# Kernel tuning notes

Hardware: AMD Instinct MI355X
Metric: run time of the kernel (lower is better)

The kernel has to match this reference:

```python
import jax, jax.numpy as jnp
import numpy as np

B = 64  # batch_size (number of graphs)


def _leaky(v):
    return jax.nn.leaky_relu(v, 0.01)


def _gine(x, src, dst, edge_attr, ew, eb, w1, b1, w2, b2):
    # GINEConv (eps=0): out = nn(x + sum_{j->i} relu(x_j + lin(edge_attr)))
    n = x.shape[0]
    msg = jax.nn.relu(x[src] + edge_attr @ ew + eb)      # [E, C]
    agg = jax.ops.segment_sum(msg, dst, num_segments=n)  # [N, C]
    h = x + agg
    h = _leaky(h @ w1 + b1)
    h = _leaky(h @ w2 + b2)
    return h


def setup_inputs() -> dict:
    key = jax.random.key(0)
    ks = jax.random.split(key, 32)
    N, E, NF, EF, H, A = 65536, 1048576, 32, 16, 128, 10
    s = 0.05
    inp = {
        'x': jax.random.normal(ks[0], (N, NF), jnp.float32),
        'edge_index': jax.random.randint(ks[1], (2, E), 0, N, jnp.int64)
        if jax.config.jax_enable_x64 else jax.random.randint(ks[1], (2, E), 0, N, jnp.int32),
        'edge_attr': jax.random.normal(ks[2], (E, EF), jnp.float32),
        'e1_w': jax.random.normal(ks[3], (EF, NF)) * s, 'e1_b': jnp.zeros((NF,)),
        'c1_w1': jax.random.normal(ks[4], (NF, H)) * s, 'c1_b1': jnp.zeros((H,)),
        'c1_w2': jax.random.normal(ks[5], (H, H)) * s, 'c1_b2': jnp.zeros((H,)),
        'e2_w': jax.random.normal(ks[6], (EF, H)) * s, 'e2_b': jnp.zeros((H,)),
        'c2_w1': jax.random.normal(ks[7], (H, H)) * s, 'c2_b1': jnp.zeros((H,)),
        'c2_w2': jax.random.normal(ks[8], (H, H)) * s, 'c2_b2': jnp.zeros((H,)),
        'a_w1': jax.random.normal(ks[9], (H, H)) * s, 'a_b1': jnp.zeros((H,)),
        'a_w2': jax.random.normal(ks[10], (H, A)) * s, 'a_b2': jnp.zeros((A,)),
        'n_w1': jax.random.normal(ks[11], (H, H)) * s, 'n_b1': jnp.zeros((H,)),
        'n_w2': jax.random.normal(ks[12], (H, H)) * s, 'n_b2': jnp.zeros((H,)),
        'n_w3': jax.random.normal(ks[13], (H, 1)) * s, 'n_b3': jnp.zeros((1,)),
    }
    return inp


def reference(x, edge_index, edge_attr,
              e1_w, e1_b, c1_w1, c1_b1, c1_w2, c1_b2,
              e2_w, e2_b, c2_w1, c2_b1, c2_w2, c2_b2,
              a_w1, a_b1, a_w2, a_b2,
              n_w1, n_b1, n_w2, n_b2, n_w3, n_b3):
    src, dst = edge_index[0], edge_index[1]
    h = _gine(x, src, dst, edge_attr, e1_w, e1_b, c1_w1, c1_b1, c1_w2, c1_b2)
    h = jax.nn.relu(h)  # dropout is identity in eval mode
    h = _gine(h, src, dst, edge_attr, e2_w, e2_b, c2_w1, c2_b1, c2_w2, c2_b2)
    H = h.shape[-1]
    hb = h.reshape(B, -1, H)            # [B, Nper, H]
    pooled = hb.mean(axis=1)            # [B, H]
    a = _leaky(_leaky(pooled @ a_w1 + a_b1) @ a_w2 + a_b2)
    action_prob = jax.nn.softmax(a, axis=1)
    # reinterpret flat node order as [Nper, B, H], as in the torch reshape
    xr = h.reshape(-1, B, H)
    nh = _leaky(xr @ n_w1 + n_b1)
    nh = _leaky(nh @ n_w2 + n_b2)
    node_scores = jax.nn.sigmoid(nh @ n_w3 + n_b3)[..., 0].T  # [B, Nper]
    return action_prob, node_scores
```

## Files before the change

kernel.cpp:

```cpp
#include <hip/hip_runtime.h>
#include <math.h>

#define NNODES 65536
#define NEDGES 1048576
#define NF 32
#define EF 16
#define HD 128
#define NACT 10
#define NB 64
#define NPER 1024

typedef unsigned short u16;
typedef float  vf2  __attribute__((ext_vector_type(2)));
typedef float  vf4  __attribute__((ext_vector_type(4)));
typedef __bf16 vbf8 __attribute__((ext_vector_type(8)));
#define BC8(v) __builtin_bit_cast(vbf8, v)
#define WB() __builtin_amdgcn_wave_barrier()

__device__ __forceinline__ float leakyf(float v) { return v > 0.0f ? v : 0.01f * v; }
__device__ __forceinline__ vf2 fma2(vf2 a, vf2 b, vf2 c) { return __builtin_elementwise_fma(a, b, c); }
__device__ __forceinline__ vf2 max2(vf2 a, vf2 b) { return __builtin_elementwise_max(a, b); }
__device__ __forceinline__ vf2 splat2(float s) { vf2 r = {s, s}; return r; }

__device__ __forceinline__ u16 f2bf(float x) {
    unsigned u = __float_as_uint(x);
    return (u16)((u + 0x7FFFu + ((u >> 16) & 1u)) >> 16);
}
__device__ __forceinline__ float bf2f(u16 h) { return __uint_as_float(((unsigned)h) << 16); }

__device__ __forceinline__ vf2 up2(unsigned d) {
    vf2 r = { __uint_as_float(d << 16), __uint_as_float(d & 0xFFFF0000u) };
    return r;
}

__device__ __forceinline__ void cvt4(const float4 s, uint2& hi, uint2& lo) {
    const u16 h0 = f2bf(s.x), h1 = f2bf(s.y), h2 = f2bf(s.z), h3 = f2bf(s.w);
    hi = make_uint2((unsigned)h0 | ((unsigned)h1 << 16), (unsigned)h2 | ((unsigned)h3 << 16));
    const u16 l0 = f2bf(s.x - bf2f(h0)), l1 = f2bf(s.y - bf2f(h1));
    const u16 l2 = f2bf(s.z - bf2f(h2)), l3 = f2bf(s.w - bf2f(h3));
    lo = make_uint2((unsigned)l0 | ((unsigned)l1 << 16), (unsigned)l2 | ((unsigned)l3 << 16));
}
__device__ __forceinline__ uint2 cvt4hi(const float4 s) {
    const u16 h0 = f2bf(s.x), h1 = f2bf(s.y), h2 = f2bf(s.z), h3 = f2bf(s.w);
    return make_uint2((unsigned)h0 | ((unsigned)h1 << 16), (unsigned)h2 | ((unsigned)h3 << 16));
}

template<int K>
__device__ __forceinline__ void bcast16_fma(const float av, const vf2* __restrict__ wr, vf2& m) {
    const float a = __uint_as_float((unsigned)__builtin_amdgcn_ds_swizzle(
        (int)__float_as_uint(av), (K << 5) | 0x10));
    m = fma2(splat2(a), wr[K], m);
    if constexpr (K + 1 < EF) bcast16_fma<K + 1>(av, wr, m);
}

__global__ __launch_bounds__(256) void hist_kernel(const int* __restrict__ ei, int* __restrict__ cnt)
{
    const int i = blockIdx.x * 256 + threadIdx.x;
    if (i < NEDGES) atomicAdd(&cnt[ei[NEDGES + i]], 1);
}

__global__ __launch_bounds__(1024) void scan_kernel(const int* __restrict__ cnt, int* __restrict__ rs)
{
    __shared__ int s[1024];
    const int t = threadIdx.x;
    int loc[64];
    int tot = 0;
    const int4* c4 = (const int4*)(cnt + t * 64);
    #pragma unroll
    for (int j = 0; j < 16; ++j) {
        const int4 v = c4[j];
        loc[4*j+0] = v.x; loc[4*j+1] = v.y; loc[4*j+2] = v.z; loc[4*j+3] = v.w;
        tot += v.x + v.y + v.z + v.w;
    }
    s[t] = tot;
    __syncthreads();
    for (int off = 1; off < 1024; off <<= 1) {
        const int v = (t >= off) ? s[t - off] : 0;
        __syncthreads();
        s[t] += v;
        __syncthreads();
    }
    int run = s[t] - tot;
    #pragma unroll
    for (int j = 0; j < 64; ++j) { rs[t * 64 + j] = run; run += loc[j]; }
    if (t == 0) rs[NNODES] = NEDGES;
}

__global__ __launch_bounds__(256) void scatter_kernel(
    const int* __restrict__ ei, const int* __restrict__ rs, int* __restrict__ fill,
    int* __restrict__ ssrc, int* __restrict__ seidx)
{
    const int i = blockIdx.x * 256 + threadIdx.x;
    if (i < NEDGES) {
        const int d = ei[NEDGES + i];
        const int pos = rs[d] + atomicAdd(&fill[d], 1);
        ssrc[pos]  = ei[i];
        seidx[pos] = i;
    }
}

__global__ __launch_bounds__(256) void permute_kernel(
    const int* __restrict__ seidx, const float* __restrict__ ea, float* __restrict__ sea)
{
    const int t = blockIdx.x * 256 + threadIdx.x;
    const int e = t >> 2, part = t & 3;
    const int idx = seidx[e];
    ((float4*)sea)[(size_t)e * 4 + part] = ((const float4*)ea)[(size_t)idx * 4 + part];
}

__global__ __launch_bounds__(256) void pack_all_kernel(
    const float* __restrict__ w0, const float* __restrict__ w1, const float* __restrict__ w2,
    const float* __restrict__ w3, const float* __restrict__ w4, const float* __restrict__ w5,
    u16* __restrict__ pw)
{
    const int bid = blockIdx.x;
    const float* W; int KB, seg, sbase;
    if (bid < 16) { W = w0; KB = 1; seg = 0; sbase = 0; }
    else {
        const int i = (bid - 16) >> 6;
        seg = i + 1; sbase = 16 + i * 64; KB = 4;
        W = (i == 0) ? w1 : (i == 1) ? w2 : (i == 2) ? w3 : (i == 3) ? w4 : w5;
    }
    const int t = (bid - sbase) * 256 + threadIdx.x;
    const int j = t & 7, lane = (t >> 3) & 63, rest = t >> 9;
    const int kb = rest % KB, fb = rest / KB;
    if (fb >= 8) return;
    const int k = kb * 32 + (lane >> 4) * 8 + j;
    const int f = fb * 16 + (lane & 15);
    const float val = W[k * HD + f];
    const u16 h = f2bf(val);
    u16* dst = pw + seg * 32768;
    dst[t] = h;
    dst[16384 + t] = f2bf(val - bf2f(h));
}

__global__ __launch_bounds__(256) void e1_agg_kernel(
    const float* __restrict__ x, const int* __restrict__ rs,
    const int* __restrict__ ssrc, const float* __restrict__ sea,
    const float* __restrict__ w, const float* __restrict__ b, float* __restrict__ agg)
{
    const int tid  = threadIdx.x;
    const int lane = tid & 63;
    const int p    = lane & 15;
    const int q    = lane >> 4;
    const int node0 = (blockIdx.x * 4 + (tid >> 6)) * 4;
    vf2 wr[EF];
    #pragma unroll
    for (int k = 0; k < EF; ++k) wr[k] = *(const vf2*)&w[k * NF + p * 2];
    const vf2 bias = *(const vf2*)&b[p * 2];
    int rsv[5];
    #pragma unroll
    for (int i = 0; i < 5; ++i) rsv[i] = __builtin_amdgcn_readfirstlane(rs[node0 + i]);
    int srcLn[4];
    #pragma unroll
    for (int n = 0; n < 4; ++n) {
        const int nw0 = min(rsv[n + 1] - rsv[n], 64);
        srcLn[n] = (lane < nw0) ? ssrc[rsv[n] + lane] : 0;
    }
    #pragma unroll
    for (int n = 0; n < 4; ++n) {
        const int beg = rsv[n], end = rsv[n + 1];
        vf2 acc = {0.0f, 0.0f};
        int srcL = srcLn[n];
        for (int wnd = beg; wnd < end; wnd += 64) {
            const int nw = min(end - wnd, 64);
            if (wnd != beg) srcL = (lane < nw) ? ssrc[wnd + lane] : 0;
            const float* sbase = sea + (size_t)wnd * EF;
            int blk = 0;
            for (; blk + 16 <= nw; blk += 16) {
                float av[4];
                #pragma unroll
                for (int u = 0; u < 4; ++u)
                    av[u] = sbase[blk * EF + u * 64 + lane];
                vf2 xv[4];
                #pragma unroll
                for (int u = 0; u < 4; ++u) {
                    const int sA = __shfl(srcL, blk + u * 4 + q, 64);
                    xv[u] = *(const vf2*)((const char*)x + (((unsigned)sA << 7) + (unsigned)p * 8));
                }
                #pragma unroll
                for (int u = 0; u < 4; ++u) {
                    vf2 m = bias;
                    bcast16_fma<0>(av[u], wr, m);
                    acc += max2(xv[u] + m, splat2(0.0f));
                }
            }
            const int nrem = nw - blk;
            if (nrem > 0) {
                #pragma unroll
                for (int u = 0; u < 4; ++u) {
                    if (u * 4 >= nrem) break;
                    const int myidx = u * 4 + q;
                    const bool valid = myidx < nrem;
                    const float av = valid ? sbase[blk * EF + u * 64 + lane] : 0.0f;
                    const int sA = __shfl(srcL, min(blk + myidx, nw - 1), 64);
                    const vf2 xv = *(const vf2*)((const char*)x + (((unsigned)sA << 7) + (unsigned)p * 8));
                    vf2 m = bias;
                    bcast16_fma<0>(av, wr, m);
                    if (valid) acc += max2(xv + m, splat2(0.0f));
                }
            }
        }
        acc[0] += __shfl_xor(acc[0], 16, 64); acc[1] += __shfl_xor(acc[1], 16, 64);
        acc[0] += __shfl_xor(acc[0], 32, 64); acc[1] += __shfl_xor(acc[1], 32, 64);
        if (lane < 16) *(vf2*)&agg[(size_t)(node0 + n) * NF + p * 2] = acc;
    }
}

__global__ __launch_bounds__(256) void e2_agg_kernel(
    const u16* __restrict__ h16, const int* __restrict__ rs,
    const int* __restrict__ ssrc, const float* __restrict__ sea,
    const float* __restrict__ w, const float* __restrict__ b, float* __restrict__ agg)
{
    const int tid  = threadIdx.x;
    const int lane = tid & 63;
    const unsigned foff = (unsigned)lane * 4;
    const int node = blockIdx.x * 4 + (tid >> 6);
    vf2 wr[EF];
    #pragma unroll
    for (int k = 0; k < EF; ++k) wr[k] = *(const vf2*)&w[k * HD + lane * 2];
    const vf2 bias = *(const vf2*)&b[lane * 2];
    const int beg = __builtin_amdgcn_readfirstlane(rs[node]);
    const int end = __builtin_amdgcn_readfirstlane(rs[node + 1]);
    vf2 acc = {0.0f, 0.0f};
    int e = beg;
    #define LDH(s) (*(const unsigned*)((const char*)h16 + (((unsigned)(s) << 8) + foff)))
    if (e + 4 <= end) {
        int s0 = ssrc[e], s1 = ssrc[e + 1], s2 = ssrc[e + 2], s3 = ssrc[e + 3];
        unsigned d0 = LDH(s0), d1 = LDH(s1), d2 = LDH(s2), d3 = LDH(s3);
        for (; e + 8 <= end; e += 4) {
            const int t0 = ssrc[e + 4], t1 = ssrc[e + 5], t2 = ssrc[e + 6], t3 = ssrc[e + 7];
            const unsigned g0 = LDH(t0), g1 = LDH(t1), g2 = LDH(t2), g3 = LDH(t3);
            const float* a0 = &sea[(size_t)e * EF];
            vf2 m0 = bias, m1 = bias, m2 = bias, m3 = bias;
            #pragma unroll
            for (int k = 0; k < EF; ++k) {
                m0 = fma2(splat2(a0[k]),      wr[k], m0);
                m1 = fma2(splat2(a0[16 + k]), wr[k], m1);
            }
            acc += max2(up2(d0) + m0, splat2(0.0f));
            acc += max2(up2(d1) + m1, splat2(0.0f));
            #pragma unroll
            for (int k = 0; k < EF; ++k) {
                m2 = fma2(splat2(a0[32 + k]), wr[k], m2);
                m3 = fma2(splat2(a0[48 + k]), wr[k], m3);
            }
            acc += max2(up2(d2) + m2, splat2(0.0f));
            acc += max2(up2(d3) + m3, splat2(0.0f));
            s0 = t0; s1 = t1; s2 = t2; s3 = t3;
            d0 = g0; d1 = g1; d2 = g2; d3 = g3;
        }
        {
            const float* a0 = &sea[(size_t)e * EF];
            vf2 m0 = bias, m1 = bias, m2 = bias, m3 = bias;
            #pragma unroll
            for (int k = 0; k < EF; ++k) {
                m0 = fma2(splat2(a0[k]),      wr[k], m0);
                m1 = fma2(splat2(a0[16 + k]), wr[k], m1);
            }
            acc += max2(up2(d0) + m0, splat2(0.0f));
            acc += max2(up2(d1) + m1, splat2(0.0f));
            #pragma unroll
            for (int k = 0; k < EF; ++k) {
                m2 = fma2(splat2(a0[32 + k]), wr[k], m2);
                m3 = fma2(splat2(a0[48 + k]), wr[k], m3);
            }
            acc += max2(up2(d2) + m2, splat2(0.0f));
            acc += max2(up2(d3) + m3, splat2(0.0f));
            e += 4;
        }
    }
    for (; e < end; ++e) {
        const int sA = ssrc[e];
        const unsigned dA = LDH(sA);
        const float* aA = &sea[(size_t)e * EF];
        vf2 mA = bias;
        #pragma unroll
        for (int k = 0; k < EF; ++k) mA = fma2(splat2(aA[k]), wr[k], mA);
        acc += max2(up2(dA) + mA, splat2(0.0f));
    }
    #undef LDH
    *(vf2*)&agg[(size_t)node * HD + lane * 2] = acc;
}

#define ROW128 272
#define ROW32  80

__device__ __forceinline__ void mfma_layer128_in(
    const unsigned char* __restrict__ aH, const unsigned char* __restrict__ aL,
    const u16* __restrict__ wH, const u16* __restrict__ wL,
    const float* __restrict__ bias, int lane, vf4* __restrict__ acc)
{
    const int quad = lane >> 4, fm = lane & 15;
    int4 Bh[4], Bl[4];
    #pragma unroll
    for (int kb = 0; kb < 4; ++kb) {
        Bh[kb] = *(const int4*)(aH + fm * ROW128 + kb * 64 + quad * 16);
        Bl[kb] = *(const int4*)(aL + fm * ROW128 + kb * 64 + quad * 16);
    }
    #pragma unroll
    for (int fb = 0; fb < 8; ++fb) {
        const float4 bv = *(const float4*)&bias[fb * 16 + quad * 4];
        vf4 a = {bv.x, bv.y, bv.z, bv.w};
        #pragma unroll
        for (int kb = 0; kb < 4; ++kb) {
            const int4 wh = *(const int4*)(wH + ((fb * 4 + kb) * 64 + lane) * 8);
            const int4 wl = *(const int4*)(wL + ((fb * 4 + kb) * 64 + lane) * 8);
            a = __builtin_amdgcn_mfma_f32_16x16x32_bf16(BC8(wh), BC8(Bl[kb]), a, 0, 0, 0);
            a = __builtin_amdgcn_mfma_f32_16x16x32_bf16(BC8(wl), BC8(Bh[kb]), a, 0, 0, 0);
            a = __builtin_amdgcn_mfma_f32_16x16x32_bf16(BC8(wh), BC8(Bh[kb]), a, 0, 0, 0);
        }
        acc[fb] = a;
    }
}

__device__ __forceinline__ void mfma_layer128_act(
    const unsigned char* __restrict__ aH,
    const u16* __restrict__ wH, const u16* __restrict__ wL,
    const float* __restrict__ bias, int lane, vf4* __restrict__ acc)
{
    const int quad = lane >> 4, fm = lane & 15;
    int4 Bh[4];
    #pragma unroll
    for (int kb = 0; kb < 4; ++kb)
        Bh[kb] = *(const int4*)(aH + fm * ROW128 + kb * 64 + quad * 16);
    #pragma unroll
    for (int fb = 0; fb < 8; ++fb) {
        const float4 bv = *(const float4*)&bias[fb * 16 + quad * 4];
        vf4 a = {bv.x, bv.y, bv.z, bv.w};
        #pragma unroll
        for (int kb = 0; kb < 4; ++kb) {
            const int4 wh = *(const int4*)(wH + ((fb * 4 + kb) * 64 + lane) * 8);
            const int4 wl = *(const int4*)(wL + ((fb * 4 + kb) * 64 + lane) * 8);
            a = __builtin_amdgcn_mfma_f32_16x16x32_bf16(BC8(wl), BC8(Bh[kb]), a, 0, 0, 0);
            a = __builtin_amdgcn_mfma_f32_16x16x32_bf16(BC8(wh), BC8(Bh[kb]), a, 0, 0, 0);
        }
        acc[fb] = a;
    }
}

__device__ __forceinline__ void mfma_layer32_in(
    const unsigned char* __restrict__ aH, const unsigned char* __restrict__ aL,
    const u16* __restrict__ wH, const u16* __restrict__ wL,
    const float* __restrict__ bias, int lane, vf4* __restrict__ acc)
{
    const int quad = lane >> 4, fm = lane & 15;
    const int4 Bh = *(const int4*)(aH + fm * ROW32 + quad * 16);
    const int4 Bl = *(const int4*)(aL + fm * ROW32 + quad * 16);
    #pragma unroll
    for (int fb = 0; fb < 8; ++fb) {
        const float4 bv = *(const float4*)&bias[fb * 16 + quad * 4];
        vf4 a = {bv.x, bv.y, bv.z, bv.w};
        const int4 wh = *(const int4*)(wH + (fb * 64 + lane) * 8);
        const int4 wl = *(const int4*)(wL + (fb * 64 + lane) * 8);
        a = __builtin_amdgcn_mfma_f32_16x16x32_bf16(BC8(wh), BC8(Bl), a, 0, 0, 0);
        a = __builtin_amdgcn_mfma_f32_16x16x32_bf16(BC8(wl), BC8(Bh), a, 0, 0, 0);
        a = __builtin_amdgcn_mfma_f32_16x16x32_bf16(BC8(wh), BC8(Bh), a, 0, 0, 0);
        acc[fb] = a;
    }
}

__device__ __forceinline__ void store_act_hi(
    unsigned char* __restrict__ aH, int lane, vf4* __restrict__ acc)
{
    const int quad = lane >> 4, fm = lane & 15;
    #pragma unroll
    for (int fb = 0; fb < 8; ++fb) {
        const float4 s = {leakyf(acc[fb][0]), leakyf(acc[fb][1]), leakyf(acc[fb][2]), leakyf(acc[fb][3])};
        acc[fb][0] = s.x; acc[fb][1] = s.y; acc[fb][2] = s.z; acc[fb][3] = s.w;
        *(uint2*)(aH + fm * ROW128 + fb * 32 + quad * 8) = cvt4hi(s);
    }
}

__global__ __launch_bounds__(256) void n1_kernel(
    const float* __restrict__ x, const float* __restrict__ agg,
    const u16* __restrict__ w1h, const u16* __restrict__ w1l, const float* __restrict__ b1,
    const u16* __restrict__ w2h, const u16* __restrict__ w2l, const float* __restrict__ b2,
    float* __restrict__ hout, u16* __restrict__ hb16)
{
    __shared__ __align__(16) unsigned char smem[4][2560 + 16 * ROW128];
    const int tid = threadIdx.x, lane = tid & 63, wid = tid >> 6;
    const int quad = lane >> 4, fm = lane & 15;
    const int tile = blockIdx.x * 4 + wid;
    unsigned char* inH = smem[wid];
    unsigned char* inL = inH + 16 * ROW32;
    unsigned char* aH  = inH + 2560;
    const size_t base = (size_t)tile * 16 * NF;
    #pragma unroll
    for (int i = 0; i < 2; ++i) {
        const int flat = i * 64 + lane;
        const int node = flat >> 3, kq = flat & 7;
        const float4 xv = *(const float4*)&x[base + node * NF + kq * 4];
        const float4 av = *(const float4*)&agg[base + node * NF + kq * 4];
        const float4 s = {xv.x + av.x, xv.y + av.y, xv.z + av.z, xv.w + av.w};
        uint2 phi, plo;
        cvt4(s, phi, plo);
        *(uint2*)(inH + node * ROW32 + kq * 8) = phi;
        *(uint2*)(inL + node * ROW32 + kq * 8) = plo;
    }
    WB();
    vf4 acc[8];
    mfma_layer32_in(inH, inL, w1h, w1l, b1, lane, acc);
    WB();
    store_act_hi(aH, lane, acc);
    WB();
    mfma_layer128_act(aH, w2h, w2l, b2, lane, acc);
    const size_t ob = (size_t)tile * 16 * HD;
    #pragma unroll
    for (int fb = 0; fb < 8; ++fb) {
        const float4 o = {fmaxf(acc[fb][0], 0.0f), fmaxf(acc[fb][1], 0.0f),
                          fmaxf(acc[fb][2], 0.0f), fmaxf(acc[fb][3], 0.0f)};
        *(float4*)&hout[ob + fm * HD + fb * 16 + quad * 4] = o;
        *(uint2*)((unsigned char*)hb16 + (((size_t)(tile * 16 + fm)) << 8) + fb * 32 + quad * 8)
            = cvt4hi(o);
    }
}

__global__ __launch_bounds__(256) void n2_kernel(
    const float* __restrict__ h, const float* __restrict__ agg,
    const u16* __restrict__ w1h, const u16* __restrict__ w1l, const float* __restrict__ b1,
    const u16* __restrict__ w2h, const u16* __restrict__ w2l, const float* __restrict__ b2,
    const u16* __restrict__ m1h, const u16* __restrict__ m1l, const float* __restrict__ nb1,
    const u16* __restrict__ m2h, const u16* __restrict__ m2l, const float* __restrict__ nb2,
    const float* __restrict__ nw3, const float* __restrict__ nb3,
    float* __restrict__ pooled, float* __restrict__ scores)
{
    __shared__ __align__(16) unsigned char smem[4][2 * 16 * ROW128];
    const int tid = threadIdx.x, lane = tid & 63, wid = tid >> 6;
    const int quad = lane >> 4, fm = lane & 15;
    const int tile = blockIdx.x * 4 + wid;
    unsigned char* aH = smem[wid];
    unsigned char* aL = aH + 16 * ROW128;
    const size_t base = (size_t)tile * 16 * HD;
    #pragma unroll
    for (int i = 0; i < 8; ++i) {
        const int flat = i * 64 + lane;
        const int node = flat >> 5, kq = flat & 31;
        const float4 hv = *(const float4*)&h[base + node * HD + kq * 4];
        const float4 av = *(const float4*)&agg[base + node * HD + kq * 4];
        const float4 s = {hv.x + av.x, hv.y + av.y, hv.z + av.z, hv.w + av.w};
        uint2 phi, plo;
        cvt4(s, phi, plo);
        *(uint2*)(aH + node * ROW128 + kq * 8) = phi;
        *(uint2*)(aL + node * ROW128 + kq * 8) = plo;
    }
    WB();
    vf4 acc[8];
    mfma_layer128_in(aH, aL, w1h, w1l, b1, lane, acc);
    WB();
    store_act_hi(aH, lane, acc);
    WB();
    mfma_layer128_act(aH, w2h, w2l, b2, lane, acc);
    WB();
    store_act_hi(aH, lane, acc);
    {
        const int g = tile >> 6;
        #pragma unroll
        for (int fb = 0; fb < 8; ++fb) {
            vf4 t = acc[fb];
            #pragma unroll
            for (int off = 1; off < 16; off <<= 1) {
                t[0] += __shfl_xor(t[0], off, 64);
                t[1] += __shfl_xor(t[1], off, 64);
                t[2] += __shfl_xor(t[2], off, 64);
                t[3] += __shfl_xor(t[3], off, 64);
            }
            #pragma unroll
            for (int r = 0; r < 4; ++r) {
                const int item = fb * 4 + r;
                if (fm == (item >> 1))
                    atomicAdd(&pooled[g * HD + fb * 16 + quad * 4 + r], t[r]);
            }
        }
    }
    WB();
    mfma_layer128_act(aH, m1h, m1l, nb1, lane, acc);
    WB();
    store_act_hi(aH, lane, acc);
    WB();
    mfma_layer128_act(aH, m2h, m2l, nb2, lane, acc);
    float v = 0.0f;
    #pragma unroll
    for (int fb = 0; fb < 8; ++fb) {
        const float4 w3v = *(const float4*)&nw3[fb * 16 + quad * 4];
        v += leakyf(acc[fb][0]) * w3v.x + leakyf(acc[fb][1]) * w3v.y
           + leakyf(acc[fb][2]) * w3v.z + leakyf(acc[fb][3]) * w3v.w;
    }
    v += __shfl_xor(v, 16, 64);
    v += __shfl_xor(v, 32, 64);
    if (lane < 16) {
        const int node = tile * 16 + fm;
        const float s = v + nb3[0];
        scores[(node & 63) * NPER + (node >> 6)] = 1.0f / (1.0f + expf(-s));
    }
}

__global__ __launch_bounds__(128) void act_kernel(
    const float* __restrict__ pooled,
    const float* __restrict__ w1, const float* __restrict__ b1,
    const float* __restrict__ w2, const float* __restrict__ b2,
    float* __restrict__ out)
{
    __shared__ __align__(16) float p[HD];
    __shared__ float a1[HD];
    __shared__ float z[NACT];
    __shared__ float red2[2];
    const int g = blockIdx.x;
    const int tid = threadIdx.x;
    p[tid] = pooled[g * HD + tid] * (1.0f / NPER);
    __syncthreads();
    float acc = b1[tid];
    for (int k = 0; k < HD; ++k) acc = fmaf(p[k], w1[k * HD + tid], acc);
    a1[tid] = leakyf(acc);
    __syncthreads();
    if (tid < NACT) {
        float a2 = b2[tid];
        for (int k = 0; k < HD; ++k) a2 = fmaf(a1[k], w2[k * NACT + tid], a2);
        z[tid] = leakyf(a2);
    }
    __syncthreads();
    if (tid == 0) {
        float m = z[0];
        for (int i = 1; i < NACT; ++i) m = fmaxf(m, z[i]);
        red2[0] = m;
    }
    __syncthreads();
    if (tid < NACT) z[tid] = expf(z[tid] - red2[0]);
    __syncthreads();
    if (tid == 0) {
        float s = 0.0f;
        for (int i = 0; i < NACT; ++i) s += z[i];
        red2[1] = s;
    }
    __syncthreads();
    if (tid < NACT) out[g * NACT + tid] = z[tid] / red2[1];
}

extern "C" void kernel_launch(void* const* d_in, const int* in_sizes, int n_in,
                              void* d_out, int out_size, void* d_ws, size_t ws_size,
                              hipStream_t stream)
{
    const float* x    = (const float*)d_in[0];
    const int*   ei   = (const int*)d_in[1];
    const float* ea   = (const float*)d_in[2];
    const float* e1w  = (const float*)d_in[3];
    const float* e1b  = (const float*)d_in[4];
    const float* c1w1 = (const float*)d_in[5];
    const float* c1b1 = (const float*)d_in[6];
    const float* c1w2 = (const float*)d_in[7];
    const float* c1b2 = (const float*)d_in[8];
    const float* e2w  = (const float*)d_in[9];
    const float* e2b  = (const float*)d_in[10];
    const float* c2w1 = (const float*)d_in[11];
    const float* c2b1 = (const float*)d_in[12];
    const float* c2w2 = (const float*)d_in[13];
    const float* c2b2 = (const float*)d_in[14];
    const float* aw1  = (const float*)d_in[15];
    const float* ab1  = (const float*)d_in[16];
    const float* aw2  = (const float*)d_in[17];
    const float* ab2  = (const float*)d_in[18];
    const float* nw1  = (const float*)d_in[19];
    const float* nb1  = (const float*)d_in[20];
    const float* nw2  = (const float*)d_in[21];
    const float* nb2  = (const float*)d_in[22];
    const float* nw3  = (const float*)d_in[23];
    const float* nb3  = (const float*)d_in[24];

    float* out = (float*)d_out;
    char*  ws  = (char*)d_ws;
    const size_t MB = 1024 * 1024;
    float* h      = (float*)(ws);
    float* agg2   = (float*)(ws + 32  * MB);
    int*   seidx  = (int*)  (ws + 32  * MB);
    float* sea    = (float*)(ws + 64  * MB);
    float* agg1   = (float*)(ws + 128 * MB);
    float* pooled = (float*)(ws + 136 * MB);
    u16*   pw     = (u16*)  (ws + 136 * MB + 64 * 1024);
    int*   cnt    = (int*)  (ws + 137 * MB);
    int*   fill   = (int*)  (ws + 137 * MB + 256 * 1024);
    int*   rs     = (int*)  (ws + 139 * MB);
    int*   ssrc   = (int*)  (ws + 140 * MB);
    u16*   hb16   = (u16*)  (ws + 144 * MB);

    u16* p_c1w1 = pw;
    u16* p_c1w2 = pw + 1 * 32768;
    u16* p_c2w1 = pw + 2 * 32768;
    u16* p_c2w2 = pw + 3 * 32768;
    u16* p_nw1  = pw + 4 * 32768;
    u16* p_nw2  = pw + 5 * 32768;

    hipMemsetAsync(cnt,    0, 2 * NNODES * sizeof(int), stream);
    hipMemsetAsync(pooled, 0, (size_t)NB * HD * sizeof(float), stream);

    pack_all_kernel<<<336, 256, 0, stream>>>(c1w1, c1w2, c2w1, c2w2, nw1, nw2, pw);

    hist_kernel<<<NEDGES / 256, 256, 0, stream>>>(ei, cnt);
    scan_kernel<<<1, 1024, 0, stream>>>(cnt, rs);
    scatter_kernel<<<NEDGES / 256, 256, 0, stream>>>(ei, rs, fill, ssrc, seidx);
    permute_kernel<<<NEDGES / 64, 256, 0, stream>>>(seidx, ea, sea);

    e1_agg_kernel<<<NNODES / 16, 256, 0, stream>>>(x, rs, ssrc, sea, e1w, e1b, agg1);
    n1_kernel<<<NNODES / 64, 256, 0, stream>>>(x, agg1,
                                               p_c1w1, p_c1w1 + 16384, c1b1,
                                               p_c1w2, p_c1w2 + 16384, c1b2, h, hb16);
    e2_agg_kernel<<<NNODES / 4, 256, 0, stream>>>(hb16, rs, ssrc, sea, e2w, e2b, agg2);
    n2_kernel<<<NNODES / 64, 256, 0, stream>>>(h, agg2,
                                               p_c2w1, p_c2w1 + 16384, c2b1,
                                               p_c2w2, p_c2w2 + 16384, c2b2,
                                               p_nw1,  p_nw1  + 16384, nb1,
                                               p_nw2,  p_nw2  + 16384, nb2,
                                               nw3, nb3, pooled, out + NB * NACT);
    act_kernel<<<NB, 128, 0, stream>>>(pooled, aw1, ab1, aw2, ab2, out);
}
```

Before: 555.3 us.

## Fuse layer-2 edge aggregation into the node MLP kernel

Moves the GINE layer-2 gather/message/segment-sum into the n2 kernel, so each wave first aggregates its 16 nodes and writes h+agg as split bf16 hi/lo straight into shared memory before the MFMA layers. This drops the agg2 round trip through global memory and one kernel launch. In exchange, the gather phase now runs with the MLP kernel's occupancy and serializes 16 nodes per wave, which may expose gather latency that the separate high-occupancy kernel used to hide.

New measurement: 609.1 us. 9.7% more time.

```diff
diff --git a/kernel.cpp b/kernel.cpp
--- a/kernel.cpp
+++ b/kernel.cpp
@@ -39,6 +39,12 @@
     const u16 l0 = f2bf(s.x - bf2f(h0)), l1 = f2bf(s.y - bf2f(h1));
     const u16 l2 = f2bf(s.z - bf2f(h2)), l3 = f2bf(s.w - bf2f(h3));
     lo = make_uint2((unsigned)l0 | ((unsigned)l1 << 16), (unsigned)l2 | ((unsigned)l3 << 16));
+}
+__device__ __forceinline__ void cvt2(const vf2 s, unsigned& hi, unsigned& lo) {
+    const u16 h0 = f2bf(s[0]), h1 = f2bf(s[1]);
+    hi = (unsigned)h0 | ((unsigned)h1 << 16);
+    const u16 l0 = f2bf(s[0] - bf2f(h0)), l1 = f2bf(s[1] - bf2f(h1));
+    lo = (unsigned)l0 | ((unsigned)l1 << 16);
 }
 __device__ __forceinline__ uint2 cvt4hi(const float4 s) {
     const u16 h0 = f2bf(s.x), h1 = f2bf(s.y), h2 = f2bf(s.z), h3 = f2bf(s.w);
@@ -207,82 +213,6 @@
     }
 }
 
-__global__ __launch_bounds__(256) void e2_agg_kernel(
-    const u16* __restrict__ h16, const int* __restrict__ rs,
-    const int* __restrict__ ssrc, const float* __restrict__ sea,
-    const float* __restrict__ w, const float* __restrict__ b, float* __restrict__ agg)
-{
-    const int tid  = threadIdx.x;
-    const int lane = tid & 63;
-    const unsigned foff = (unsigned)lane * 4;
-    const int node = blockIdx.x * 4 + (tid >> 6);
-    vf2 wr[EF];
-    #pragma unroll
-    for (int k = 0; k < EF; ++k) wr[k] = *(const vf2*)&w[k * HD + lane * 2];
-    const vf2 bias = *(const vf2*)&b[lane * 2];
-    const int beg = __builtin_amdgcn_readfirstlane(rs[node]);
-    const int end = __builtin_amdgcn_readfirstlane(rs[node + 1]);
-    vf2 acc = {0.0f, 0.0f};
-    int e = beg;
-    #define LDH(s) (*(const unsigned*)((const char*)h16 + (((unsigned)(s) << 8) + foff)))
-    if (e + 4 <= end) {
-        int s0 = ssrc[e], s1 = ssrc[e + 1], s2 = ssrc[e + 2], s3 = ssrc[e + 3];
-        unsigned d0 = LDH(s0), d1 = LDH(s1), d2 = LDH(s2), d3 = LDH(s3);
-        for (; e + 8 <= end; e += 4) {
-            const int t0 = ssrc[e + 4], t1 = ssrc[e + 5], t2 = ssrc[e + 6], t3 = ssrc[e + 7];
-            const unsigned g0 = LDH(t0), g1 = LDH(t1), g2 = LDH(t2), g3 = LDH(t3);
-            const float* a0 = &sea[(size_t)e * EF];
-            vf2 m0 = bias, m1 = bias, m2 = bias, m3 = bias;
-            #pragma unroll
-            for (int k = 0; k < EF; ++k) {
-                m0 = fma2(splat2(a0[k]),      wr[k], m0);
-                m1 = fma2(splat2(a0[16 + k]), wr[k], m1);
-            }
-            acc += max2(up2(d0) + m0, splat2(0.0f));
-            acc += max2(up2(d1) + m1, splat2(0.0f));
-            #pragma unroll
-            for (int k = 0; k < EF; ++k) {
-                m2 = fma2(splat2(a0[32 + k]), wr[k], m2);
-                m3 = fma2(splat2(a0[48 + k]), wr[k], m3);
-            }
-            acc += max2(up2(d2) + m2, splat2(0.0f));
-            acc += max2(up2(d3) + m3, splat2(0.0f));
-            s0 = t0; s1 = t1; s2 = t2; s3 = t3;
-            d0 = g0; d1 = g1; d2 = g2; d3 = g3;
-        }
-        {
-            const float* a0 = &sea[(size_t)e * EF];
-            vf2 m0 = bias, m1 = bias, m2 = bias, m3 = bias;
-            #pragma unroll
-            for (int k = 0; k < EF; ++k) {
-                m0 = fma2(splat2(a0[k]),      wr[k], m0);
-                m1 = fma2(splat2(a0[16 + k]), wr[k], m1);
-            }
-            acc += max2(up2(d0) + m0, splat2(0.0f));
-            acc += max2(up2(d1) + m1, splat2(0.0f));
-            #pragma unroll
-            for (int k = 0; k < EF; ++k) {
-                m2 = fma2(splat2(a0[32 + k]), wr[k], m2);
-                m3 = fma2(splat2(a0[48 + k]), wr[k], m3);
-            }
-            acc += max2(up2(d2) + m2, splat2(0.0f));
-            acc += max2(up2(d3) + m3, splat2(0.0f));
-            e += 4;
-        }
-    }
-    for (; e < end; ++e) {
-        const int sA = ssrc[e];
-        const unsigned dA = LDH(sA);
-        const float* aA = &sea[(size_t)e * EF];
-        vf2 mA = bias;
-        #pragma unroll
-        for (int k = 0; k < EF; ++k) mA = fma2(splat2(aA[k]), wr[k], mA);
-        acc += max2(up2(dA) + mA, splat2(0.0f));
-    }
-    #undef LDH
-    *(vf2*)&agg[(size_t)node * HD + lane * 2] = acc;
-}
-
 #define ROW128 272
 #define ROW32  80
 
@@ -416,8 +346,10 @@
     }
 }
 
-__global__ __launch_bounds__(256) void n2_kernel(
-    const float* __restrict__ h, const float* __restrict__ agg,
+__global__ __launch_bounds__(256) void en2_kernel(
+    const float* __restrict__ h, const u16* __restrict__ h16,
+    const int* __restrict__ rs, const int* __restrict__ ssrc, const float* __restrict__ sea,
+    const float* __restrict__ ew, const float* __restrict__ eb,
     const u16* __restrict__ w1h, const u16* __restrict__ w1l, const float* __restrict__ b1,
     const u16* __restrict__ w2h, const u16* __restrict__ w2l, const float* __restrict__ b2,
     const u16* __restrict__ m1h, const u16* __restrict__ m1l, const float* __restrict__ nb1,
@@ -431,18 +363,82 @@
     const int tile = blockIdx.x * 4 + wid;
     unsigned char* aH = smem[wid];
     unsigned char* aL = aH + 16 * ROW128;
-    const size_t base = (size_t)tile * 16 * HD;
-    #pragma unroll
-    for (int i = 0; i < 8; ++i) {
-        const int flat = i * 64 + lane;
-        const int node = flat >> 5, kq = flat & 31;
-        const float4 hv = *(const float4*)&h[base + node * HD + kq * 4];
-        const float4 av = *(const float4*)&agg[base + node * HD + kq * 4];
-        const float4 s = {hv.x + av.x, hv.y + av.y, hv.z + av.z, hv.w + av.w};
-        uint2 phi, plo;
-        cvt4(s, phi, plo);
-        *(uint2*)(aH + node * ROW128 + kq * 8) = phi;
-        *(uint2*)(aL + node * ROW128 + kq * 8) = plo;
+
+    {
+        vf2 wr[EF];
+        #pragma unroll
+        for (int k = 0; k < EF; ++k) wr[k] = *(const vf2*)&ew[k * HD + lane * 2];
+        const vf2 ebias = *(const vf2*)&eb[lane * 2];
+        const unsigned foff = (unsigned)lane * 4;
+        const int node0 = tile * 16;
+        #define LDH(s) (*(const unsigned*)((const char*)h16 + (((unsigned)(s) << 8) + foff)))
+        for (int n = 0; n < 16; ++n) {
+            const int beg = __builtin_amdgcn_readfirstlane(rs[node0 + n]);
+            const int end = __builtin_amdgcn_readfirstlane(rs[node0 + n + 1]);
+            vf2 acc = {0.0f, 0.0f};
+            int e = beg;
+            if (e + 4 <= end) {
+                int s0 = ssrc[e], s1 = ssrc[e + 1], s2 = ssrc[e + 2], s3 = ssrc[e + 3];
+                unsigned d0 = LDH(s0), d1 = LDH(s1), d2 = LDH(s2), d3 = LDH(s3);
+                for (; e + 8 <= end; e += 4) {
+                    const int t0 = ssrc[e + 4], t1 = ssrc[e + 5], t2 = ssrc[e + 6], t3 = ssrc[e + 7];
+                    const unsigned g0 = LDH(t0), g1 = LDH(t1), g2 = LDH(t2), g3 = LDH(t3);
+                    const float* a0 = &sea[(size_t)e * EF];
+                    vf2 m0 = ebias, m1 = ebias, m2 = ebias, m3 = ebias;
+                    #pragma unroll
+                    for (int k = 0; k < EF; ++k) {
+                        m0 = fma2(splat2(a0[k]),      wr[k], m0);
+                        m1 = fma2(splat2(a0[16 + k]), wr[k], m1);
+                    }
+                    acc += max2(up2(d0) + m0, splat2(0.0f));
+                    acc += max2(up2(d1) + m1, splat2(0.0f));
+                    #pragma unroll
+                    for (int k = 0; k < EF; ++k) {
+                        m2 = fma2(splat2(a0[32 + k]), wr[k], m2);
+                        m3 = fma2(splat2(a0[48 + k]), wr[k], m3);
+                    }
+                    acc += max2(up2(d2) + m2, splat2(0.0f));
+                    acc += max2(up2(d3) + m3, splat2(0.0f));
+                    s0 = t0; s1 = t1; s2 = t2; s3 = t3;
+                    d0 = g0; d1 = g1; d2 = g2; d3 = g3;
+                }
+                {
+                    const float* a0 = &sea[(size_t)e * EF];
+                    vf2 m0 = ebias, m1 = ebias, m2 = ebias, m3 = ebias;
+                    #pragma unroll
+                    for (int k = 0; k < EF; ++k) {
+                        m0 = fma2(splat2(a0[k]),      wr[k], m0);
+                        m1 = fma2(splat2(a0[16 + k]), wr[k], m1);
+                    }
+                    acc += max2(up2(d0) + m0, splat2(0.0f));
+                    acc += max2(up2(d1) + m1, splat2(0.0f));
+                    #pragma unroll
+                    for (int k = 0; k < EF; ++k) {
+                        m2 = fma2(splat2(a0[32 + k]), wr[k], m2);
+                        m3 = fma2(splat2(a0[48 + k]), wr[k], m3);
+                    }
+                    acc += max2(up2(d2) + m2, splat2(0.0f));
+                    acc += max2(up2(d3) + m3, splat2(0.0f));
+                    e += 4;
+                }
+            }
+            for (; e < end; ++e) {
+                const int sA = ssrc[e];
+                const unsigned dA = LDH(sA);
+                const float* aA = &sea[(size_t)e * EF];
+                vf2 mA = ebias;
+                #pragma unroll
+                for (int k = 0; k < EF; ++k) mA = fma2(splat2(aA[k]), wr[k], mA);
+                acc += max2(up2(dA) + mA, splat2(0.0f));
+            }
+            const vf2 hv = *(const vf2*)&h[((size_t)(node0 + n)) * HD + lane * 2];
+            const vf2 s = hv + acc;
+            unsigned phi, plo;
+            cvt2(s, phi, plo);
+            *(unsigned*)(aH + n * ROW128 + lane * 4) = phi;
+            *(unsigned*)(aL + n * ROW128 + lane * 4) = plo;
+        }
+        #undef LDH
     }
     WB();
     vf4 acc[8];
@@ -570,7 +566,6 @@
     char*  ws  = (char*)d_ws;
     const size_t MB = 1024 * 1024;
     float* h      = (float*)(ws);
-    float* agg2   = (float*)(ws + 32  * MB);
     int*   seidx  = (int*)  (ws + 32  * MB);
     float* sea    = (float*)(ws + 64  * MB);
     float* agg1   = (float*)(ws + 128 * MB);
@@ -603,12 +598,11 @@
     n1_kernel<<<NNODES / 64, 256, 0, stream>>>(x, agg1,
                                                p_c1w1, p_c1w1 + 16384, c1b1,
                                                p_c1w2, p_c1w2 + 16384, c1b2, h, hb16);
-    e2_agg_kernel<<<NNODES / 4, 256, 0, stream>>>(hb16, rs, ssrc, sea, e2w, e2b, agg2);
-    n2_kernel<<<NNODES / 64, 256, 0, stream>>>(h, agg2,
-                                               p_c2w1, p_c2w1 + 16384, c2b1,
-                                               p_c2w2, p_c2w2 + 16384, c2b2,
-                                               p_nw1,  p_nw1  + 16384, nb1,
-                                               p_nw2,  p_nw2  + 16384, nb2,
-                                               nw3, nb3, pooled, out + NB * NACT);
+    en2_kernel<<<NNODES / 64, 256, 0, stream>>>(h, hb16, rs, ssrc, sea, e2w, e2b,
+                                                p_c2w1, p_c2w1 + 16384, c2b1,
+                                                p_c2w2, p_c2w2 + 16384, c2b2,
+                                                p_nw1,  p_nw1  + 16384, nb1,
+                                                p_nw2,  p_nw2  + 16384, nb2,
+                                                nw3, nb3, pooled, out + NB * NACT);
     act_kernel<<<NB, 128, 0, stream>>>(pooled, aw1, ab1, aw2, ab2, out);
 }
```
